# Performance work log

Hardware: AMD Instinct MI355X
Metric: run time of the kernel (lower is better)

## Reference

```python
import jax, jax.numpy as jnp
import numpy as np


def setup_inputs() -> dict:
    key = jax.random.key(0)
    k1, k2, k3, k4 = jax.random.split(key, 4)
    B, L, D = 16, 2048, 128
    return {
        "query": jax.random.normal(k1, (B, L, D), dtype=jnp.float32),
        "key": jax.random.normal(k2, (B, L, D), dtype=jnp.float32),
        "value": jax.random.normal(k3, (B, L, D), dtype=jnp.float32),
        "mask": jax.random.randint(k4, (B, L, L), 0, 2, dtype=jnp.int32),
    }


def reference(query, key, value, mask):
    # scores: [B, L_q, L_k], scaled by sqrt(D_q)
    scale = 1.0 / jnp.sqrt(jnp.asarray(query.shape[-1], dtype=query.dtype))
    scores = jnp.einsum("bqd,bkd->bqk", query, key) * scale
    NEG = jnp.asarray(-1e9, dtype=scores.dtype)
    scores = jnp.where(mask == 0, NEG, scores)
    p_attn = jax.nn.softmax(scores, axis=-1)
    context = jnp.einsum("bqk,bkd->bqd", p_attn, value)
    return (context, p_attn)
```

## Files before the change

kernel.cpp:

```cpp
#include <hip/hip_runtime.h>
#include <hip/hip_bf16.h>
#include <hip/hip_fp16.h>

#define BB 16
#define LL 2048
#define DD 128
#define SCALE 0.08838834764831845f
#define CEXP 12.0f
#define NT 32

typedef _Float16 f16x8 __attribute__((ext_vector_type(8)));
typedef float f32x16 __attribute__((ext_vector_type(16)));

#define MFMA32(a,b,c) __builtin_amdgcn_mfma_f32_32x32x16_f16((a),(b),(c),0,0,0)

#define OFF_KB   0
#define OFF_VB   65536
#define OFF_PB   131072
#define OFF_RED  147456
#define LDS_MAIN 148480

#define WAITVM(N)  asm volatile("s_waitcnt vmcnt(" #N ")" ::: "memory")
#define WAITLGKM0  asm volatile("s_waitcnt lgkmcnt(0)" ::: "memory")
#define MEMFENCE   asm volatile("" ::: "memory")
#define SB0        __builtin_amdgcn_sched_barrier(0)

__device__ __forceinline__ f16x8 as_f16x8(uint4 v){
  union { uint4 u; f16x8 h; } x; x.u = v; return x.h;
}
__device__ __forceinline__ unsigned pkf16(float a, float b){
  __half ha = __float2half_rn(a), hb = __float2half_rn(b);
  return (unsigned)__half_as_ushort(ha) | ((unsigned)__half_as_ushort(hb) << 16);
}
__device__ __forceinline__ unsigned pkrtz(float a, float b){
  union { decltype(__builtin_amdgcn_cvt_pkrtz(0.f, 0.f)) h; unsigned u; } x;
  x.h = __builtin_amdgcn_cvt_pkrtz(a, b);
  return x.u;
}
__device__ __forceinline__ void stage16(const unsigned char* g, char* l){
  __builtin_amdgcn_global_load_lds(
      (const __attribute__((address_space(1))) void*)g,
      (__attribute__((address_space(3))) void*)l, 16, 0, 0);
}
__device__ __forceinline__ void stage2(const unsigned char* g, char* l, int soff){
  stage16(g + soff, l + soff);
  stage16(g + soff + 1024, l + soff + 1024);
}

__global__ __launch_bounds__(256) void prep_all(
    const float* __restrict__ K, const float* __restrict__ V,
    const int* __restrict__ M,
    unsigned char* __restrict__ kimg, unsigned char* __restrict__ vimg,
    unsigned int* __restrict__ bm)
{
  __shared__ float t[32][65];
  const int bid = blockIdx.x, tid = threadIdx.x;
  if (bid < 8192) {
    const size_t wi = (size_t)bid * 256 + tid;
    const int* mp = M + wi * 32;
    unsigned int wrd = 0;
#pragma unroll
    for (int j = 0; j < 8; ++j) {
      int4 v = *(const int4*)(mp + j*4);
      wrd |= (v.x ? 1u : 0u) << (4*j)
          |  (v.y ? 1u : 0u) << (4*j+1)
          |  (v.z ? 1u : 0u) << (4*j+2)
          |  (v.w ? 1u : 0u) << (4*j+3);
    }
    bm[wi] = wrd;
  } else if (bid < 10240) {
    const int G = (bid - 8192)*256 + tid;
    const int b = G >> 15;
    const int k = (G >> 4) & 2047;
    const int gd = G & 15;
    const float* src = K + ((size_t)b*LL + k)*DD + gd*8;
    float4 f0 = *(const float4*)(src);
    float4 f1 = *(const float4*)(src + 4);
    uint4 o;
    o.x = pkf16(f0.x, f0.y); o.y = pkf16(f0.z, f0.w);
    o.z = pkf16(f1.x, f1.y); o.w = pkf16(f1.z, f1.w);
    const size_t base = ((size_t)b*NT + (k>>6))*16384;
    *(uint4*)(kimg + base + (k&63)*256 + ((gd*16) ^ ((k&15)<<4))) = o;
  } else {
    const int t2 = bid - 10240;
    const int b = t2 >> 7;
    const int rem = t2 & 127;
    const int kt = rem >> 2, dt = rem & 3;
    const int k0 = kt*64, d0 = dt*32;
    const int kl = tid >> 2, dq = (tid & 3)*8;
    const float* src = V + ((size_t)b*LL + k0 + kl)*DD + d0 + dq;
    float4 f0 = *(const float4*)(src);
    float4 f1 = *(const float4*)(src + 4);
    t[dq+0][kl] = f0.x; t[dq+1][kl] = f0.y; t[dq+2][kl] = f0.z; t[dq+3][kl] = f0.w;
    t[dq+4][kl] = f1.x; t[dq+5][kl] = f1.y; t[dq+6][kl] = f1.z; t[dq+7][kl] = f1.w;
    __syncthreads();
    const int dl = tid >> 3, kg = tid & 7;
    const int d = d0 + dl;
    uint4 o;
    o.x = pkf16(t[dl][kg*8+0], t[dl][kg*8+1]);
    o.y = pkf16(t[dl][kg*8+2], t[dl][kg*8+3]);
    o.z = pkf16(t[dl][kg*8+4], t[dl][kg*8+5]);
    o.w = pkf16(t[dl][kg*8+6], t[dl][kg*8+7]);
    const size_t base = ((size_t)b*NT + kt)*16384;
    *(uint4*)(vimg + base + d*128 + ((kg*16) ^ ((d&7)<<4))) = o;
  }
}

#define QKCOMPUTE(BUFIDX) \
  const char* kb = KB + (BUFIDX)*16384 + krow*256; \
  f32x16 aA, aB; \
  _Pragma("unroll") for (int i=0;i<16;++i){aA[i]=0.f;aB[i]=0.f;} \
  _Pragma("unroll") for (int s=0;s<4;++s){ \
    uint4 af = *(const uint4*)(kb + (((s*2+hi)*16) ^ kswz)); \
    aA = MFMA32(as_f16x8(af), as_f16x8(qf[s]), aA); } \
  _Pragma("unroll") for (int s=4;s<8;++s){ \
    uint4 af = *(const uint4*)(kb + (((s*2+hi)*16) ^ kswz)); \
    aB = MFMA32(as_f16x8(af), as_f16x8(qf[s]), aB); }

#define P1BODY(RR) do { \
  WAITVM(6); \
  __builtin_amdgcn_s_barrier(); \
  MEMFENCE; \
  const unsigned bn2 = BMl[2*(((RR)+2)&31)]; \
  SB0; \
  stage2(KIMG + imgb + (size_t)(((RR)+3)&31)*16384, KB + (((RR)+3)&3)*16384, soff); \
  SB0; \
  QKCOMPUTE((RR)&3); \
  const unsigned bwh = bcur >> (4*hi); \
  _Pragma("unroll") for (int i=0;i<16;++i){ \
    const float sv = ((bwh>>((i&3)+8*(i>>2)))&1u) ? fmaf(aA[i]+aB[i], SCALE, -CEXP) : -1.0e9f; \
    psum[i&3] += __expf(sv); } \
  bcur = bn1; bn1 = bn2; \
} while(0)

#define P2BODY(RR, NTOK) do { \
  WAITVM(NTOK); \
  __builtin_amdgcn_s_barrier(); \
  MEMFENCE; \
  const unsigned bn2 = BMl[2*(((RR)+2)&31)]; \
  SB0; \
  stage2(KIMG + imgb + (size_t)(((RR)+3)&31)*16384, KB + (((RR)+3)&3)*16384, soff); \
  stage2(VIMG + imgb + (size_t)(((RR)+3)&31)*16384, VB + (((RR)+3)&3)*16384, soff); \
  SB0; \
  QKCOMPUTE((RR)&3); \
  const unsigned bwh = bcur >> (4*hi); \
  float pv[16]; \
  _Pragma("unroll") for (int i=0;i<16;++i){ \
    const float sv = ((bwh>>((i&3)+8*(i>>2)))&1u) ? fmaf(aA[i]+aB[i], SCALE, -CEXP) : -1.0e9f; \
    pv[i] = __expf(sv) * inv; } \
  { float* pr = Prow + (size_t)(RR)*64 + sub*32 + hi*4; \
    float4 o; \
    o.x=pv[0];  o.y=pv[1];  o.z=pv[2];  o.w=pv[3];  *(float4*)(pr)    = o; \
    o.x=pv[4];  o.y=pv[5];  o.z=pv[6];  o.w=pv[7];  *(float4*)(pr+8)  = o; \
    o.x=pv[8];  o.y=pv[9];  o.z=pv[10]; o.w=pv[11]; *(float4*)(pr+16) = o; \
    o.x=pv[12]; o.y=pv[13]; o.z=pv[14]; o.w=pv[15]; *(float4*)(pr+24) = o; } \
  SB0; \
  { char* pb = PB + p*4096 + sub*2048; \
    uint2 u; \
    u.x = pkrtz(pv[0],pv[1]);   u.y = pkrtz(pv[2],pv[3]);   *(uint2*)(pb + c*16 + hi*8) = u; \
    u.x = pkrtz(pv[4],pv[5]);   u.y = pkrtz(pv[6],pv[7]);   *(uint2*)(pb + (c+32)*16 + hi*8) = u; \
    u.x = pkrtz(pv[8],pv[9]);   u.y = pkrtz(pv[10],pv[11]); *(uint2*)(pb + 1024 + c*16 + hi*8) = u; \
    u.x = pkrtz(pv[12],pv[13]); u.y = pkrtz(pv[14],pv[15]); *(uint2*)(pb + 1024 + (c+32)*16 + hi*8) = u; } \
  WAITLGKM0; \
  __builtin_amdgcn_s_barrier(); \
  MEMFENCE; \
  _Pragma("unroll") for (int s2=0;s2<2;++s2){ \
    _Pragma("unroll") for (int k2=0;k2<2;++k2){ \
      const uint4 afr = *(const uint4*)(PB + p*4096 + s2*2048 + k2*1024 + l*16); \
      const int gix = s2*4 + k2*2 + hi; \
      const int d0v = sub*64 + c; \
      const uint4 b0 = *(const uint4*)(VB + ((RR)&3)*16384 + d0v*128 + ((gix*16) ^ ((d0v&7)<<4))); \
      ctx0 = MFMA32(as_f16x8(afr), as_f16x8(b0), ctx0); \
      const int d1v = sub*64 + 32 + c; \
      const uint4 b1 = *(const uint4*)(VB + ((RR)&3)*16384 + d1v*128 + ((gix*16) ^ ((d1v&7)<<4))); \
      ctx1 = MFMA32(as_f16x8(afr), as_f16x8(b1), ctx1); } } \
  bcur = bn1; bn1 = bn2; \
} while(0)

__global__ __launch_bounds__(512) void attn_main(
    const float* __restrict__ Q, const unsigned int* __restrict__ BM,
    const unsigned char* __restrict__ KIMG, const unsigned char* __restrict__ VIMG,
    float* __restrict__ ctxout, float* __restrict__ pout)
{
  extern __shared__ char lds[];
  char* KB = lds + OFF_KB;
  char* VB = lds + OFF_VB;
  char* PB = lds + OFF_PB;
  float* RED = (float*)(lds + OFF_RED);

  const int tid = threadIdx.x;
  const int w = tid >> 6, l = tid & 63;
  const int c = l & 31, hi = l >> 5;
  const int p = w >> 1, sub = w & 1;

  const int bid = blockIdx.x;
  const int xcd = bid & 7, jj = bid >> 3;
  const int b = xcd*2 + (jj >> 4);
  const int q0 = (jj & 15) * 128;
  const int qrow = q0 + p*32 + c;

  uint4 qf[8];
  const float* qp0 = Q + ((size_t)b*LL + qrow)*DD;
#pragma unroll
  for (int s = 0; s < 8; ++s) {
    const float4 f0 = *(const float4*)(qp0 + s*16 + hi*8);
    const float4 f1 = *(const float4*)(qp0 + s*16 + hi*8 + 4);
    uint4 qv;
    qv.x = pkf16(f0.x, f0.y); qv.y = pkf16(f0.z, f0.w);
    qv.z = pkf16(f1.x, f1.y); qv.w = pkf16(f1.z, f1.w);
    qf[s] = qv;
  }

  const size_t imgb = ((size_t)b * NT) * 16384;
  const int soff = w*2048 + l*16;
  const unsigned int* BMl = BM + ((size_t)b*LL + qrow)*64 + sub;
  const int krow = sub*32 + c;
  const int kswz = (c & 15) << 4;

  stage2(KIMG + imgb + 0*16384, KB + 0*16384, soff); SB0;
  unsigned bcur = BMl[0]; SB0;
  stage2(KIMG + imgb + 1*16384, KB + 1*16384, soff); SB0;
  unsigned bn1 = BMl[2]; SB0;
  stage2(KIMG + imgb + 2*16384, KB + 2*16384, soff); SB0;

  float psum[4] = {0.f, 0.f, 0.f, 0.f};
#pragma unroll 1
  for (int r = 0; r < 32; ++r) {
    P1BODY(r);
  }
  float sum = (psum[0] + psum[1]) + (psum[2] + psum[3]);
  sum += __shfl_xor(sum, 32);
  __syncthreads();
  if (l < 32) RED[(p*2+sub)*32 + c] = sum;
  __syncthreads();
  float tot = RED[(p*2+sub)*32 + c] + RED[(p*2+(1-sub))*32 + c];
  tot = fmaxf(tot, 1e-35f);
  const float inv = 1.0f / tot;
  __syncthreads();

  stage2(KIMG + imgb + 0*16384, KB + 0*16384, soff);
  stage2(VIMG + imgb + 0*16384, VB + 0*16384, soff); SB0;
  bcur = BMl[0]; SB0;
  stage2(KIMG + imgb + 1*16384, KB + 1*16384, soff);
  stage2(VIMG + imgb + 1*16384, VB + 1*16384, soff); SB0;
  bn1 = BMl[2]; SB0;
  stage2(KIMG + imgb + 2*16384, KB + 2*16384, soff);
  stage2(VIMG + imgb + 2*16384, VB + 2*16384, soff); SB0;

  f32x16 ctx0, ctx1;
#pragma unroll
  for (int i = 0; i < 16; ++i) { ctx0[i] = 0.f; ctx1[i] = 0.f; }
  float* Prow = pout + ((size_t)b*LL + qrow)*LL;

  P2BODY(0, 10);
  P2BODY(1, 14);
  P2BODY(2, 18);
#pragma unroll 1
  for (int r = 3; r < 32; ++r) {
    P2BODY(r, 22);
  }

#pragma unroll
  for (int reg = 0; reg < 16; ++reg) {
    const int q = q0 + p*32 + (reg&3) + 8*(reg>>2) + 4*hi;
    float* cr = ctxout + ((size_t)b*LL + q)*DD;
    cr[sub*64 + c]      = ctx0[reg];
    cr[sub*64 + 32 + c] = ctx1[reg];
  }
}

__global__ __launch_bounds__(256) void attn_naive(
    const float* __restrict__ Q, const float* __restrict__ K,
    const float* __restrict__ V, const int* __restrict__ M,
    float* __restrict__ ctx, float* __restrict__ pout)
{
  const int b = blockIdx.x >> 11;
  const int q = blockIdx.x & (LL-1);
  __shared__ float s[LL];
  __shared__ float red[256];
  const int tid = threadIdx.x;
  const float* qp = Q + ((size_t)b*LL + q)*DD;
  for (int kk = tid; kk < LL; kk += 256) {
    const float* kp = K + ((size_t)b*LL + kk)*DD;
    float a = 0.f;
    for (int d = 0; d < DD; ++d) a += qp[d]*kp[d];
    s[kk] = M[((size_t)b*LL + q)*LL + kk] ? a*SCALE : -1e9f;
  }
  __syncthreads();
  float mx = -3e38f;
  for (int kk = tid; kk < LL; kk += 256) mx = fmaxf(mx, s[kk]);
  red[tid] = mx; __syncthreads();
  for (int o = 128; o >= 1; o >>= 1) {
    if (tid < o) red[tid] = fmaxf(red[tid], red[tid+o]);
    __syncthreads();
  }
  const float mrow = red[0]; __syncthreads();
  float sm = 0.f;
  for (int kk = tid; kk < LL; kk += 256) { float e = __expf(s[kk]-mrow); s[kk] = e; sm += e; }
  red[tid] = sm; __syncthreads();
  for (int o = 128; o >= 1; o >>= 1) {
    if (tid < o) red[tid] += red[tid+o];
    __syncthreads();
  }
  const float inv = 1.0f / red[0]; __syncthreads();
  float* prow = pout + ((size_t)b*LL + q)*LL;
  for (int kk = tid; kk < LL; kk += 256) { s[kk] *= inv; prow[kk] = s[kk]; }
  __syncthreads();
  if (tid < DD) {
    float a = 0.f;
    for (int kk = 0; kk < LL; ++kk) a += s[kk]*V[((size_t)b*LL + kk)*DD + tid];
    ctx[((size_t)b*LL + q)*DD + tid] = a;
  }
}

extern "C" void kernel_launch(void* const* d_in, const int* in_sizes, int n_in,
                              void* d_out, int out_size, void* d_ws, size_t ws_size,
                              hipStream_t stream) {
  (void)in_sizes; (void)n_in; (void)out_size;
  const float* Q = (const float*)d_in[0];
  const float* K = (const float*)d_in[1];
  const float* V = (const float*)d_in[2];
  const int*   M = (const int*)d_in[3];
  float* ctx  = (float*)d_out;
  float* pout = ctx + (size_t)BB*LL*DD;
  const size_t IMG = (size_t)BB*NT*16384;
  const size_t NBM = (size_t)BB*LL*(LL/32);
  const size_t WS_NEED = IMG*2 + NBM*4;
  if (ws_size >= WS_NEED) {
    unsigned char* kimg = (unsigned char*)d_ws;
    unsigned char* vimg = kimg + IMG;
    unsigned int*  bmw  = (unsigned int*)(vimg + IMG);
    hipFuncSetAttribute(reinterpret_cast<const void*>(attn_main),
                        hipFuncAttributeMaxDynamicSharedMemorySize, LDS_MAIN);
    prep_all<<<12288, 256, 0, stream>>>(K, V, M, kimg, vimg, bmw);
    attn_main<<<256, 512, LDS_MAIN, stream>>>(Q, bmw, kimg, vimg, ctx, pout);
  } else {
    attn_naive<<<BB*LL, 256, 0, stream>>>(Q, K, V, M, ctx, pout);
  }
}
```

Baseline: 202.3 us.

## Split softmax-denominator pass into separate kernel fused with mask bit-packing

Moves the first (row-sum) pass out of the main attention kernel into a separate kernel that also reads the int32 mask directly, packs it into bitmask words, and writes per-row sums. The main kernel then loads the precomputed sums instead of recomputing QK^T over all keys. This removes the separate mask-packing work from the prep kernel and lets pass 1 run with a different grid (512 blocks, no LDS staging, direct global K loads) for better occupancy. It adds one kernel launch and a global round-trip for the sums, and pass 1 now loads K from global memory without LDS reuse.

```diff
diff --git a/kernel.cpp b/kernel.cpp
--- a/kernel.cpp
+++ b/kernel.cpp
@@ -17,8 +17,7 @@
 #define OFF_KB   0
 #define OFF_VB   65536
 #define OFF_PB   131072
-#define OFF_RED  147456
-#define LDS_MAIN 148480
+#define LDS_MAIN 147456
 
 #define WAITVM(N)  asm volatile("s_waitcnt vmcnt(" #N ")" ::: "memory")
 #define WAITLGKM0  asm volatile("s_waitcnt lgkmcnt(0)" ::: "memory")
@@ -47,29 +46,14 @@
   stage16(g + soff + 1024, l + soff + 1024);
 }
 
-__global__ __launch_bounds__(256) void prep_all(
+__global__ __launch_bounds__(256) void prep_kv(
     const float* __restrict__ K, const float* __restrict__ V,
-    const int* __restrict__ M,
-    unsigned char* __restrict__ kimg, unsigned char* __restrict__ vimg,
-    unsigned int* __restrict__ bm)
+    unsigned char* __restrict__ kimg, unsigned char* __restrict__ vimg)
 {
   __shared__ float t[32][65];
   const int bid = blockIdx.x, tid = threadIdx.x;
-  if (bid < 8192) {
-    const size_t wi = (size_t)bid * 256 + tid;
-    const int* mp = M + wi * 32;
-    unsigned int wrd = 0;
-#pragma unroll
-    for (int j = 0; j < 8; ++j) {
-      int4 v = *(const int4*)(mp + j*4);
-      wrd |= (v.x ? 1u : 0u) << (4*j)
-          |  (v.y ? 1u : 0u) << (4*j+1)
-          |  (v.z ? 1u : 0u) << (4*j+2)
-          |  (v.w ? 1u : 0u) << (4*j+3);
-    }
-    bm[wi] = wrd;
-  } else if (bid < 10240) {
-    const int G = (bid - 8192)*256 + tid;
+  if (bid < 2048) {
+    const int G = bid*256 + tid;
     const int b = G >> 15;
     const int k = (G >> 4) & 2047;
     const int gd = G & 15;
@@ -82,7 +66,7 @@
     const size_t base = ((size_t)b*NT + (k>>6))*16384;
     *(uint4*)(kimg + base + (k&63)*256 + ((gd*16) ^ ((k&15)<<4))) = o;
   } else {
-    const int t2 = bid - 10240;
+    const int t2 = bid - 2048;
     const int b = t2 >> 7;
     const int rem = t2 & 127;
     const int kt = rem >> 2, dt = rem & 3;
@@ -106,6 +90,84 @@
   }
 }
 
+__global__ __launch_bounds__(512, 4) void pass1(
+    const float* __restrict__ Q, const int* __restrict__ M,
+    const unsigned char* __restrict__ KIMG,
+    unsigned int* __restrict__ BM, float* __restrict__ Sums)
+{
+  __shared__ float RED[2][4][32];
+  const int tid = threadIdx.x;
+  const int w = tid >> 6, l = tid & 63;
+  const int c = l & 31, hi = l >> 5;
+  const int p = w >> 2, ww = w & 3;
+
+  const int bid = blockIdx.x;
+  const int xcd = bid & 7, jj = bid >> 3;
+  const int b = xcd*2 + (jj >> 5);
+  const int q0 = (jj & 31) * 64;
+  const int qrow = q0 + p*32 + c;
+
+  uint4 qf[8];
+  const float* qp0 = Q + ((size_t)b*LL + qrow)*DD;
+#pragma unroll
+  for (int s = 0; s < 8; ++s) {
+    const float4 f0 = *(const float4*)(qp0 + s*16 + hi*8);
+    const float4 f1 = *(const float4*)(qp0 + s*16 + hi*8 + 4);
+    uint4 qv;
+    qv.x = pkf16(f0.x, f0.y); qv.y = pkf16(f0.z, f0.w);
+    qv.z = pkf16(f1.x, f1.y); qv.w = pkf16(f1.z, f1.w);
+    qf[s] = qv;
+  }
+
+  const size_t imgb = ((size_t)b * NT) * 16384;
+  const int kswz = (c & 15) << 4;
+  const int* Mrow = M + ((size_t)b*LL + qrow)*LL;
+  const size_t bmrow = ((size_t)b*LL + qrow)*64;
+
+  float psum[4] = {0.f, 0.f, 0.f, 0.f};
+#pragma unroll 4
+  for (int t = 0; t < 16; ++t) {
+    const int kbase = ww*512 + t*32;
+    const int tile  = kbase >> 6;
+    const int sub2  = (kbase >> 5) & 1;
+    const unsigned char* kbg = KIMG + imgb + (size_t)tile*16384 + (sub2*32 + c)*256;
+    uint4 kf[8];
+#pragma unroll
+    for (int s = 0; s < 8; ++s)
+      kf[s] = *(const uint4*)(kbg + (((s*2+hi)*16) ^ kswz));
+    const int4 m0 = *(const int4*)(Mrow + kbase + hi*4);
+    const int4 m1 = *(const int4*)(Mrow + kbase + hi*4 + 8);
+    const int4 m2 = *(const int4*)(Mrow + kbase + hi*4 + 16);
+    const int4 m3 = *(const int4*)(Mrow + kbase + hi*4 + 24);
+    f32x16 acc;
+#pragma unroll
+    for (int i = 0; i < 16; ++i) acc[i] = 0.f;
+#pragma unroll
+    for (int s = 0; s < 8; ++s) acc = MFMA32(as_f16x8(kf[s]), as_f16x8(qf[s]), acc);
+    const unsigned w16 = (m0.x?0x1u:0u)|(m0.y?0x2u:0u)|(m0.z?0x4u:0u)|(m0.w?0x8u:0u)
+                       | (m1.x?0x100u:0u)|(m1.y?0x200u:0u)|(m1.z?0x400u:0u)|(m1.w?0x800u:0u)
+                       | (m2.x?0x10000u:0u)|(m2.y?0x20000u:0u)|(m2.z?0x40000u:0u)|(m2.w?0x80000u:0u)
+                       | (m3.x?0x1000000u:0u)|(m3.y?0x2000000u:0u)|(m3.z?0x4000000u:0u)|(m3.w?0x8000000u:0u);
+    const unsigned pw = __shfl_xor(w16, 32);
+    if (l < 32) BM[bmrow + ww*16 + t] = w16 | (pw << 4);
+#pragma unroll
+    for (int i = 0; i < 16; ++i) {
+      const float sv = ((w16>>((i&3)+8*(i>>2)))&1u) ? fmaf(acc[i], SCALE, -CEXP) : -1.0e9f;
+      psum[i&3] += __expf(sv);
+    }
+  }
+  float s = (psum[0] + psum[1]) + (psum[2] + psum[3]);
+  s += __shfl_xor(s, 32);
+  if (l < 32) RED[p][ww][c] = s;
+  __syncthreads();
+  if (tid < 64) {
+    const int p2 = tid >> 5, c2 = tid & 31;
+    const float tot = (RED[p2][0][c2] + RED[p2][1][c2])
+                    + (RED[p2][2][c2] + RED[p2][3][c2]);
+    Sums[(size_t)b*LL + q0 + p2*32 + c2] = tot;
+  }
+}
+
 #define QKCOMPUTE(BUFIDX) \
   const char* kb = KB + (BUFIDX)*16384 + krow*256; \
   f32x16 aA, aB; \
@@ -116,22 +178,6 @@
   _Pragma("unroll") for (int s=4;s<8;++s){ \
     uint4 af = *(const uint4*)(kb + (((s*2+hi)*16) ^ kswz)); \
     aB = MFMA32(as_f16x8(af), as_f16x8(qf[s]), aB); }
-
-#define P1BODY(RR) do { \
-  WAITVM(6); \
-  __builtin_amdgcn_s_barrier(); \
-  MEMFENCE; \
-  const unsigned bn2 = BMl[2*(((RR)+2)&31)]; \
-  SB0; \
-  stage2(KIMG + imgb + (size_t)(((RR)+3)&31)*16384, KB + (((RR)+3)&3)*16384, soff); \
-  SB0; \
-  QKCOMPUTE((RR)&3); \
-  const unsigned bwh = bcur >> (4*hi); \
-  _Pragma("unroll") for (int i=0;i<16;++i){ \
-    const float sv = ((bwh>>((i&3)+8*(i>>2)))&1u) ? fmaf(aA[i]+aB[i], SCALE, -CEXP) : -1.0e9f; \
-    psum[i&3] += __expf(sv); } \
-  bcur = bn1; bn1 = bn2; \
-} while(0)
 
 #define P2BODY(RR, NTOK) do { \
   WAITVM(NTOK); \
@@ -177,8 +223,9 @@
   bcur = bn1; bn1 = bn2; \
 } while(0)
 
-__global__ __launch_bounds__(512) void attn_main(
+__global__ __launch_bounds__(512) void pass2(
     const float* __restrict__ Q, const unsigned int* __restrict__ BM,
+    const float* __restrict__ Sums,
     const unsigned char* __restrict__ KIMG, const unsigned char* __restrict__ VIMG,
     float* __restrict__ ctxout, float* __restrict__ pout)
 {
@@ -186,7 +233,6 @@
   char* KB = lds + OFF_KB;
   char* VB = lds + OFF_VB;
   char* PB = lds + OFF_PB;
-  float* RED = (float*)(lds + OFF_RED);
 
   const int tid = threadIdx.x;
   const int w = tid >> 6, l = tid & 63;
@@ -217,33 +263,15 @@
   const int krow = sub*32 + c;
   const int kswz = (c & 15) << 4;
 
-  stage2(KIMG + imgb + 0*16384, KB + 0*16384, soff); SB0;
-  unsigned bcur = BMl[0]; SB0;
-  stage2(KIMG + imgb + 1*16384, KB + 1*16384, soff); SB0;
-  unsigned bn1 = BMl[2]; SB0;
-  stage2(KIMG + imgb + 2*16384, KB + 2*16384, soff); SB0;
-
-  float psum[4] = {0.f, 0.f, 0.f, 0.f};
-#pragma unroll 1
-  for (int r = 0; r < 32; ++r) {
-    P1BODY(r);
-  }
-  float sum = (psum[0] + psum[1]) + (psum[2] + psum[3]);
-  sum += __shfl_xor(sum, 32);
-  __syncthreads();
-  if (l < 32) RED[(p*2+sub)*32 + c] = sum;
-  __syncthreads();
-  float tot = RED[(p*2+sub)*32 + c] + RED[(p*2+(1-sub))*32 + c];
-  tot = fmaxf(tot, 1e-35f);
-  const float inv = 1.0f / tot;
-  __syncthreads();
+  const float tot = Sums[(size_t)b*LL + qrow];
+  const float inv = 1.0f / fmaxf(tot, 1e-35f);
 
   stage2(KIMG + imgb + 0*16384, KB + 0*16384, soff);
   stage2(VIMG + imgb + 0*16384, VB + 0*16384, soff); SB0;
-  bcur = BMl[0]; SB0;
+  unsigned bcur = BMl[0]; SB0;
   stage2(KIMG + imgb + 1*16384, KB + 1*16384, soff);
   stage2(VIMG + imgb + 1*16384, VB + 1*16384, soff); SB0;
-  bn1 = BMl[2]; SB0;
+  unsigned bn1 = BMl[2]; SB0;
   stage2(KIMG + imgb + 2*16384, KB + 2*16384, soff);
   stage2(VIMG + imgb + 2*16384, VB + 2*16384, soff); SB0;
 
@@ -325,15 +353,18 @@
   float* pout = ctx + (size_t)BB*LL*DD;
   const size_t IMG = (size_t)BB*NT*16384;
   const size_t NBM = (size_t)BB*LL*(LL/32);
-  const size_t WS_NEED = IMG*2 + NBM*4;
+  const size_t NSUM = (size_t)BB*LL;
+  const size_t WS_NEED = IMG*2 + NBM*4 + NSUM*4;
   if (ws_size >= WS_NEED) {
     unsigned char* kimg = (unsigned char*)d_ws;
     unsigned char* vimg = kimg + IMG;
     unsigned int*  bmw  = (unsigned int*)(vimg + IMG);
-    hipFuncSetAttribute(reinterpret_cast<const void*>(attn_main),
+    float*         sums = (float*)(bmw + NBM);
+    hipFuncSetAttribute(reinterpret_cast<const void*>(pass2),
                         hipFuncAttributeMaxDynamicSharedMemorySize, LDS_MAIN);
-    prep_all<<<12288, 256, 0, stream>>>(K, V, M, kimg, vimg, bmw);
-    attn_main<<<256, 512, LDS_MAIN, stream>>>(Q, bmw, kimg, vimg, ctx, pout);
+    prep_kv<<<4096, 256, 0, stream>>>(K, V, kimg, vimg);
+    pass1<<<512, 512, 0, stream>>>(Q, M, kimg, bmw, sums);
+    pass2<<<256, 512, LDS_MAIN, stream>>>(Q, bmw, sums, kimg, vimg, ctx, pout);
   } else {
     attn_naive<<<BB*LL, 256, 0, stream>>>(Q, K, V, M, ctx, pout);
   }
```

After: 443.6 us. +119.2%, slower.

## Build PV operand in registers via permlane32 swap, drop LDS P staging and barrier

Applied to the files above, without the earlier changes.

Replaces the per-iteration write of the probability tile to LDS, the wait and the block barrier, and the LDS reread with a register-only permlane32_swap that turns the QK MFMA output into the A operand of the PV MFMA. Each wave now covers all 128 output dims for its own key half, using four accumulators instead of two. The two halves are summed through LDS once at the end. This removes a barrier and LDS traffic from every key block, at the cost of twice the accumulator registers, twice the V loads per wave and a final reduction step.

```diff
diff --git a/kernel.cpp b/kernel.cpp
--- a/kernel.cpp
+++ b/kernel.cpp
@@ -16,12 +16,10 @@
 
 #define OFF_KB   0
 #define OFF_VB   65536
-#define OFF_PB   131072
 #define OFF_RED  147456
 #define LDS_MAIN 148480
 
 #define WAITVM(N)  asm volatile("s_waitcnt vmcnt(" #N ")" ::: "memory")
-#define WAITLGKM0  asm volatile("s_waitcnt lgkmcnt(0)" ::: "memory")
 #define MEMFENCE   asm volatile("" ::: "memory")
 #define SB0        __builtin_amdgcn_sched_barrier(0)
 
@@ -36,6 +34,13 @@
   union { decltype(__builtin_amdgcn_cvt_pkrtz(0.f, 0.f)) h; unsigned u; } x;
   x.h = __builtin_amdgcn_cvt_pkrtz(a, b);
   return x.u;
+}
+__device__ __forceinline__ void pl32swap(unsigned a, unsigned b,
+                                         unsigned* ra, unsigned* rb){
+  union { decltype(__builtin_amdgcn_permlane32_swap(0u, 0u, false, false)) v;
+          uint2 u; } x;
+  x.v = __builtin_amdgcn_permlane32_swap(a, b, false, false);
+  *ra = x.u.x; *rb = x.u.y;
 }
 __device__ __forceinline__ void stage16(const unsigned char* g, char* l){
   __builtin_amdgcn_global_load_lds(
@@ -155,25 +160,25 @@
     o.x=pv[8];  o.y=pv[9];  o.z=pv[10]; o.w=pv[11]; *(float4*)(pr+16) = o; \
     o.x=pv[12]; o.y=pv[13]; o.z=pv[14]; o.w=pv[15]; *(float4*)(pr+24) = o; } \
   SB0; \
-  { char* pb = PB + p*4096 + sub*2048; \
-    uint2 u; \
-    u.x = pkrtz(pv[0],pv[1]);   u.y = pkrtz(pv[2],pv[3]);   *(uint2*)(pb + c*16 + hi*8) = u; \
-    u.x = pkrtz(pv[4],pv[5]);   u.y = pkrtz(pv[6],pv[7]);   *(uint2*)(pb + (c+32)*16 + hi*8) = u; \
-    u.x = pkrtz(pv[8],pv[9]);   u.y = pkrtz(pv[10],pv[11]); *(uint2*)(pb + 1024 + c*16 + hi*8) = u; \
-    u.x = pkrtz(pv[12],pv[13]); u.y = pkrtz(pv[14],pv[15]); *(uint2*)(pb + 1024 + (c+32)*16 + hi*8) = u; } \
-  WAITLGKM0; \
-  __builtin_amdgcn_s_barrier(); \
-  MEMFENCE; \
-  _Pragma("unroll") for (int s2=0;s2<2;++s2){ \
-    _Pragma("unroll") for (int k2=0;k2<2;++k2){ \
-      const uint4 afr = *(const uint4*)(PB + p*4096 + s2*2048 + k2*1024 + l*16); \
-      const int gix = s2*4 + k2*2 + hi; \
-      const int d0v = sub*64 + c; \
-      const uint4 b0 = *(const uint4*)(VB + ((RR)&3)*16384 + d0v*128 + ((gix*16) ^ ((d0v&7)<<4))); \
-      ctx0 = MFMA32(as_f16x8(afr), as_f16x8(b0), ctx0); \
-      const int d1v = sub*64 + 32 + c; \
-      const uint4 b1 = *(const uint4*)(VB + ((RR)&3)*16384 + d1v*128 + ((gix*16) ^ ((d1v&7)<<4))); \
-      ctx1 = MFMA32(as_f16x8(afr), as_f16x8(b1), ctx1); } } \
+  uint4 af0, af1; \
+  { unsigned r0a, r0b, r1a, r1b; \
+    pl32swap(pkrtz(pv[0],pv[1]), pkrtz(pv[4],pv[5]), &r0a, &r0b); \
+    pl32swap(pkrtz(pv[2],pv[3]), pkrtz(pv[6],pv[7]), &r1a, &r1b); \
+    af0.x = r0a; af0.y = r1a; af0.z = r0b; af0.w = r1b; \
+    pl32swap(pkrtz(pv[8],pv[9]),  pkrtz(pv[12],pv[13]), &r0a, &r0b); \
+    pl32swap(pkrtz(pv[10],pv[11]), pkrtz(pv[14],pv[15]), &r1a, &r1b); \
+    af1.x = r0a; af1.y = r1a; af1.z = r0b; af1.w = r1b; } \
+  { const char* vbb = VB + ((RR)&3)*16384; \
+    const int d0v = 0*32 + c, d1v = 1*32 + c, d2v = 2*32 + c, d3v = 3*32 + c; \
+    const int g0 = sub*4 + hi, g1 = sub*4 + 2 + hi; \
+    acc0 = MFMA32(as_f16x8(af0), as_f16x8(*(const uint4*)(vbb + d0v*128 + ((g0*16) ^ ((d0v&7)<<4)))), acc0); \
+    acc1 = MFMA32(as_f16x8(af0), as_f16x8(*(const uint4*)(vbb + d1v*128 + ((g0*16) ^ ((d1v&7)<<4)))), acc1); \
+    acc2 = MFMA32(as_f16x8(af0), as_f16x8(*(const uint4*)(vbb + d2v*128 + ((g0*16) ^ ((d2v&7)<<4)))), acc2); \
+    acc3 = MFMA32(as_f16x8(af0), as_f16x8(*(const uint4*)(vbb + d3v*128 + ((g0*16) ^ ((d3v&7)<<4)))), acc3); \
+    acc0 = MFMA32(as_f16x8(af1), as_f16x8(*(const uint4*)(vbb + d0v*128 + ((g1*16) ^ ((d0v&7)<<4)))), acc0); \
+    acc1 = MFMA32(as_f16x8(af1), as_f16x8(*(const uint4*)(vbb + d1v*128 + ((g1*16) ^ ((d1v&7)<<4)))), acc1); \
+    acc2 = MFMA32(as_f16x8(af1), as_f16x8(*(const uint4*)(vbb + d2v*128 + ((g1*16) ^ ((d2v&7)<<4)))), acc2); \
+    acc3 = MFMA32(as_f16x8(af1), as_f16x8(*(const uint4*)(vbb + d3v*128 + ((g1*16) ^ ((d3v&7)<<4)))), acc3); } \
   bcur = bn1; bn1 = bn2; \
 } while(0)
 
@@ -185,7 +190,6 @@
   extern __shared__ char lds[];
   char* KB = lds + OFF_KB;
   char* VB = lds + OFF_VB;
-  char* PB = lds + OFF_PB;
   float* RED = (float*)(lds + OFF_RED);
 
   const int tid = threadIdx.x;
@@ -247,9 +251,9 @@
   stage2(KIMG + imgb + 2*16384, KB + 2*16384, soff);
   stage2(VIMG + imgb + 2*16384, VB + 2*16384, soff); SB0;
 
-  f32x16 ctx0, ctx1;
-#pragma unroll
-  for (int i = 0; i < 16; ++i) { ctx0[i] = 0.f; ctx1[i] = 0.f; }
+  f32x16 acc0, acc1, acc2, acc3;
+#pragma unroll
+  for (int i = 0; i < 16; ++i) { acc0[i] = 0.f; acc1[i] = 0.f; acc2[i] = 0.f; acc3[i] = 0.f; }
   float* Prow = pout + ((size_t)b*LL + qrow)*LL;
 
   P2BODY(0, 10);
@@ -260,12 +264,29 @@
     P2BODY(r, 22);
   }
 
-#pragma unroll
-  for (int reg = 0; reg < 16; ++reg) {
-    const int q = q0 + p*32 + (reg&3) + 8*(reg>>2) + 4*hi;
-    float* cr = ctxout + ((size_t)b*LL + q)*DD;
-    cr[sub*64 + c]      = ctx0[reg];
-    cr[sub*64 + 32 + c] = ctx1[reg];
+  WAITVM(0);
+  __syncthreads();
+  float* xch = (float*)(lds + OFF_KB);
+  if (sub == 1) {
+#pragma unroll
+    for (int i = 0; i < 16; ++i) {
+      xch[p*4096 + 0*1024 + i*64 + l] = acc0[i];
+      xch[p*4096 + 1*1024 + i*64 + l] = acc1[i];
+      xch[p*4096 + 2*1024 + i*64 + l] = acc2[i];
+      xch[p*4096 + 3*1024 + i*64 + l] = acc3[i];
+    }
+  }
+  __syncthreads();
+  if (sub == 0) {
+#pragma unroll
+    for (int i = 0; i < 16; ++i) {
+      const int q = q0 + p*32 + (i&3) + 8*(i>>2) + 4*hi;
+      float* cr = ctxout + ((size_t)b*LL + q)*DD;
+      cr[0*32 + c] = acc0[i] + xch[p*4096 + 0*1024 + i*64 + l];
+      cr[1*32 + c] = acc1[i] + xch[p*4096 + 1*1024 + i*64 + l];
+      cr[2*32 + c] = acc2[i] + xch[p*4096 + 2*1024 + i*64 + l];
+      cr[3*32 + c] = acc3[i] + xch[p*4096 + 3*1024 + i*64 + l];
+    }
   }
 }
 
```

Measured after the change: 203.7 us. Within noise of the previous version (+0.7%).
